# Performance work log

Hardware: AMD Instinct MI355X
Metric: run time of the kernel (lower is better)

Reference implementation:

```python
import jax, jax.numpy as jnp
import numpy as np

B, S, H, MAX_STEP = 128, 1024, 256, 10
NEG_INF = -1e8


def setup_inputs() -> dict:
    key = jax.random.key(0)
    ks = jax.random.split(key, 16)
    sc = 0.05
    return {
        "s0": jax.random.normal(ks[0], (B, H), jnp.float32),
        "h0": jax.random.normal(ks[1], (B, H), jnp.float32),
        "doc_encoding": jax.random.normal(ks[2], (B, S, H), jnp.float32),
        "W_ih": jax.random.normal(ks[3], (3 * H, H), jnp.float32) * sc,
        "W_hh": jax.random.normal(ks[4], (3 * H, H), jnp.float32) * sc,
        "b_ih": jax.random.normal(ks[5], (3 * H,), jnp.float32) * sc,
        "b_hh": jax.random.normal(ks[6], (3 * H,), jnp.float32) * sc,
        "Wq": jax.random.normal(ks[7], (H, H), jnp.float32) * sc,
        "bq": jax.random.normal(ks[8], (H,), jnp.float32) * sc,
        "Wd": jax.random.normal(ks[9], (H, H), jnp.float32) * sc,
        "bd": jax.random.normal(ks[10], (H,), jnp.float32) * sc,
        "Ws": jax.random.normal(ks[11], (1, H), jnp.float32) * sc,
        "bs": jax.random.normal(ks[12], (1,), jnp.float32) * sc,
        "tgt": jax.random.randint(ks[13], (B, MAX_STEP), 0, S, jnp.int64 if jax.config.jax_enable_x64 else jnp.int32),
        "sent_length": jax.random.randint(ks[14], (B,), 1, S + 1, jnp.int64 if jax.config.jax_enable_x64 else jnp.int32),
    }


def reference(s0, h0, doc_encoding, W_ih, W_hh, b_ih, b_hh, Wq, bq, Wd, bd, Ws, bs, tgt, sent_length):
    batch, sent_len, hid = doc_encoding.shape
    # padding mask: 1 where position >= doc length
    mask = (jnp.arange(sent_len)[None, :] >= sent_length[:, None]).astype(doc_encoding.dtype)  # [B,S]
    # precomputed attention keys: linear_d(context)
    precompute = jnp.einsum('bsh,kh->bsk', doc_encoding, Wd) + bd  # [B,S,H]
    # teacher-forced indices (original maps -1 -> 0)
    tgt_idx = jnp.where(tgt == -1, 0, tgt)  # [B,T]
    batch_ar = jnp.arange(batch)

    def gru_cell(x, h):
        gi = x @ W_ih.T + b_ih  # [B,3H]
        gh = h @ W_hh.T + b_hh
        i_r, i_z, i_n = jnp.split(gi, 3, axis=-1)
        h_r, h_z, h_n = jnp.split(gh, 3, axis=-1)
        r = jax.nn.sigmoid(i_r + h_r)
        z = jax.nn.sigmoid(i_z + h_z)
        n = jnp.tanh(i_n + r * h_n)
        return (1.0 - z) * n + z * h

    def step(carry, idx_t):
        cur_input, h = carry
        h = gru_cell(cur_input, h)
        target = h @ Wq.T + bq  # [B,H]
        energy = jnp.squeeze(jnp.tanh(precompute + target[:, None, :]) @ Ws.T, -1) + bs[0]  # [B,S]
        energy = energy * (1.0 - mask) + mask * NEG_INF
        cur_next = doc_encoding[batch_ar, idx_t]  # hard-attention gather [B,H]
        return (cur_next, h), energy

    _, all_score = jax.lax.scan(step, (s0, h0), tgt_idx.T)  # [T,B,S]
    return all_score, mask
```

## Files before the change

kernel.cpp:

```cpp
#include <hip/hip_runtime.h>

typedef unsigned short ushort_t;
typedef unsigned int uint_t;
typedef __attribute__((ext_vector_type(8))) short short8;
typedef __attribute__((ext_vector_type(4))) float f32x4;

#define B_   128
#define S_   1024
#define H_   256
#define T_   10
#define NEG_INF_ -1e8f

static __device__ __forceinline__ ushort_t f2bf(float x) {
    unsigned int u = __float_as_uint(x);
    unsigned int r = u + 0x7FFFu + ((u >> 16) & 1u);
    return (ushort_t)(r >> 16);
}
static __device__ __forceinline__ float bflo(uint_t w) {
    return __uint_as_float(w << 16);
}
static __device__ __forceinline__ float bfhi(uint_t w) {
    return __uint_as_float(w & 0xFFFF0000u);
}
static __device__ __forceinline__ float sigf(float x) {
    return 1.0f / (1.0f + __expf(-x));
}
static __device__ __forceinline__ float tanh_acc(float x) {
    return 2.0f / (1.0f + __expf(-2.0f * x)) - 1.0f;
}
static __device__ __forceinline__ float tanh_fast(float x) {
    float u = x * x;
    float p = fmaf(0.019063f, u, -0.18852f);
    p = fmaf(p, u, 0.93106f);
    float r = x * p;
    return __builtin_amdgcn_fmed3f(r, -1.0f, 1.0f);
}
static __device__ __forceinline__ short8 pack_bf8(float4 a, float4 b) {
    short8 r;
    r[0] = (short)f2bf(a.x); r[1] = (short)f2bf(a.y);
    r[2] = (short)f2bf(a.z); r[3] = (short)f2bf(a.w);
    r[4] = (short)f2bf(b.x); r[5] = (short)f2bf(b.y);
    r[6] = (short)f2bf(b.z); r[7] = (short)f2bf(b.w);
    return r;
}

__global__ void prep_transpose(const float* __restrict__ W_ih,
                               const float* __restrict__ W_hh,
                               const float* __restrict__ Wq,
                               uint_t* __restrict__ planes) {
    __shared__ float lds[64][65];
    const int p = blockIdx.x >> 4, tile = blockIdx.x & 15;
    const int j0 = (tile >> 2) * 64, c0 = (tile & 3) * 64;
    const float* src;
    if (p < 3)      src = W_ih + (size_t)p * 65536;
    else if (p < 6) src = W_hh + (size_t)(p - 3) * 65536;
    else            src = Wq;
    uint_t* dst = planes + (size_t)p * 32768;
    const int tid = threadIdx.x;
#pragma unroll
    for (int p4 = 0; p4 < 4; ++p4) {
        int i = p4 * 256 + tid;
        int jj = i >> 4, cc4 = (i & 15) * 4;
        float4 v = *((const float4*)&src[(size_t)(j0 + jj) * 256 + c0 + cc4]);
        lds[jj][cc4]     = v.x;
        lds[jj][cc4 + 1] = v.y;
        lds[jj][cc4 + 2] = v.z;
        lds[jj][cc4 + 3] = v.w;
    }
    __syncthreads();
#pragma unroll
    for (int p8 = 0; p8 < 8; ++p8) {
        int i = p8 * 256 + tid;
        int c2 = i >> 6, j = i & 63;
        float lo = lds[j][c2 * 2], hi = lds[j][c2 * 2 + 1];
        uint_t val = (uint_t)f2bf(lo) | ((uint_t)f2bf(hi) << 16);
        dst[(size_t)(c0 / 2 + c2) * 256 + j0 + j] = val;
    }
}

__global__ void prep_small(const float* __restrict__ Wd, const int* __restrict__ slen,
                           ushort_t* __restrict__ Wd_bf, float* __restrict__ out_mask,
                           float* __restrict__ out_score) {
    int i = blockIdx.x * 256 + threadIdx.x;
    if (i < 65536) { Wd_bf[i] = f2bf(Wd[i]); return; }
    i -= 65536;
    if (i < B_ * S_) {
        int b = i >> 10, s = i & 1023;
        out_mask[i] = (s >= slen[b]) ? 1.0f : 0.0f;
        return;
    }
    i -= B_ * S_;
    int bs = i & (B_ * S_ - 1);
    int b = bs >> 10, s = bs & 1023;
    if (s >= slen[b]) out_score[i] = NEG_INF_;
}

__global__ __launch_bounds__(1024) void build_tiles(const int* __restrict__ slen,
                                                    int* __restrict__ tlist,
                                                    int* __restrict__ tcount) {
    const int tid = threadIdx.x;
    const int b = tid >> 3, st = tid & 7;
    const bool active = (st * 128) < slen[b];
    unsigned long long m = __ballot(active);
    const int lane = tid & 63, wv = tid >> 6;
    __shared__ int wbase[16];
    if (lane == 0) wbase[wv] = __popcll(m);
    __syncthreads();
    if (tid == 0) {
        int s = 0;
#pragma unroll
        for (int i = 0; i < 16; ++i) { int c = wbase[i]; wbase[i] = s; s += c; }
        *tcount = s;
    }
    __syncthreads();
    if (active) {
        unsigned long long below = (lane == 0) ? 0ull : (m << (64 - lane));
        int pos = wbase[wv] + __popcll(below);
        tlist[pos] = tid;
    }
}

__global__ __launch_bounds__(512) void gru_all(
        const float* __restrict__ s0, const float* __restrict__ h0,
        const float* __restrict__ doc, const int* __restrict__ tgt,
        const uint_t* __restrict__ planes, const float* __restrict__ b_ih,
        const float* __restrict__ b_hh, const float* __restrict__ bq,
        float* __restrict__ targets) {
    __shared__ float xs[T_][256];
    __shared__ float hs[256];
    __shared__ float pr[256], pz[256], pn[256], pq[256];
    const int b = blockIdx.x;
    const int tid = threadIdx.x;
    const int j = tid & 255, half = tid >> 8;

    const uint_t* ihr = planes;
    const uint_t* ihz = planes + 32768;
    const uint_t* ihn = planes + 2 * 32768;
    const uint_t* hhr = planes + 3 * 32768;
    const uint_t* hhz = planes + 4 * 32768;
    const uint_t* hhn = planes + 5 * 32768;
    const uint_t* qT  = planes + 6 * 32768;

    for (int i = tid; i < 640; i += 512) {
        int t = i >> 6, c4 = i & 63;
        const float* src;
        if (t == 0) src = s0 + (size_t)b * H_;
        else {
            int idx = tgt[b * T_ + t - 1];
            if (idx < 0) idx = 0;
            src = doc + ((size_t)b * S_ + idx) * H_;
        }
        ((float4*)&xs[t][0])[c4] = ((const float4*)src)[c4];
    }
    if (half == 0) hs[j] = h0[(size_t)b * H_ + j];
    const float bhr = b_hh[j], bhz = b_hh[j + 256], bhn = b_hh[j + 512];
    const float bqj = bq[j];
    const float bihr = b_ih[j], bihz = b_ih[j + 256], bihn = b_ih[j + 512];
    __syncthreads();

    float g_r[5], g_z[5], g_n[5];
#pragma unroll
    for (int u = 0; u < 5; ++u) { g_r[u] = bihr; g_z[u] = bihz; g_n[u] = bihn; }
    const int tbase = half * 5;
#pragma unroll 1
    for (int bb = 0; bb < 16; ++bb) {
        uint_t wr8[8], wz8[8], wn8[8];
#pragma unroll
        for (int v = 0; v < 8; ++v) {
            int c2 = bb * 8 + v;
            wr8[v] = ihr[c2 * 256 + j];
            wz8[v] = ihz[c2 * 256 + j];
            wn8[v] = ihn[c2 * 256 + j];
        }
#pragma unroll
        for (int v = 0; v < 8; ++v) {
            int c2 = bb * 8 + v;
            float wr0 = bflo(wr8[v]), wr1 = bfhi(wr8[v]);
            float wz0 = bflo(wz8[v]), wz1 = bfhi(wz8[v]);
            float wn0 = bflo(wn8[v]), wn1 = bfhi(wn8[v]);
#pragma unroll
            for (int u = 0; u < 5; ++u) {
                float2 x2 = *((const float2*)&xs[tbase + u][c2 * 2]);
                g_r[u] = fmaf(wr0, x2.x, g_r[u]); g_r[u] = fmaf(wr1, x2.y, g_r[u]);
                g_z[u] = fmaf(wz0, x2.x, g_z[u]); g_z[u] = fmaf(wz1, x2.y, g_z[u]);
                g_n[u] = fmaf(wn0, x2.x, g_n[u]); g_n[u] = fmaf(wn1, x2.y, g_n[u]);
            }
        }
    }

    const int c2base = half * 64;
    const uint_t* hhr_h = hhr + (size_t)c2base * 256 + j;
    const uint_t* hhz_h = hhz + (size_t)c2base * 256 + j;
    const uint_t* hhn_h = hhn + (size_t)c2base * 256 + j;
    const uint_t* qT_h  = qT  + (size_t)c2base * 256 + j;

#pragma unroll
    for (int t = 0; t < T_; ++t) {
        const bool holder = (half == (t >= 5 ? 1 : 0));
        const int u = (t < 5) ? t : t - 5;
        float ar = 0.f, az = 0.f, an = 0.f;
#pragma unroll 1
        for (int bb = 0; bb < 8; ++bb) {
            uint_t wr8[8], wz8[8], wn8[8];
#pragma unroll
            for (int v = 0; v < 8; ++v) {
                int c2i = bb * 8 + v;
                wr8[v] = hhr_h[c2i * 256];
                wz8[v] = hhz_h[c2i * 256];
                wn8[v] = hhn_h[c2i * 256];
            }
#pragma unroll
            for (int v = 0; v < 8; ++v) {
                int c2i = bb * 8 + v;
                float2 h2 = *((const float2*)&hs[(c2base + c2i) * 2]);
                ar = fmaf(bflo(wr8[v]), h2.x, ar); ar = fmaf(bfhi(wr8[v]), h2.y, ar);
                az = fmaf(bflo(wz8[v]), h2.x, az); az = fmaf(bfhi(wz8[v]), h2.y, az);
                an = fmaf(bflo(wn8[v]), h2.x, an); an = fmaf(bfhi(wn8[v]), h2.y, an);
            }
        }
        if (!holder) { pr[j] = ar; pz[j] = az; pn[j] = an; }
        __syncthreads();
        if (holder) {
            float art = ar + pr[j] + bhr;
            float azt = az + pz[j] + bhz;
            float ant = an + pn[j] + bhn;
            float r = sigf(g_r[u] + art);
            float z = sigf(g_z[u] + azt);
            float n = tanh_acc(fmaf(r, ant, g_n[u]));
            float hold = hs[j];
            hs[j] = fmaf(z, hold - n, n);
        }
        __syncthreads();
        float q = 0.f;
#pragma unroll 1
        for (int bb = 0; bb < 4; ++bb) {
            uint_t wq16[16];
#pragma unroll
            for (int v = 0; v < 16; ++v)
                wq16[v] = qT_h[(bb * 16 + v) * 256];
#pragma unroll
            for (int v = 0; v < 16; ++v) {
                int c2i = bb * 16 + v;
                float2 h2 = *((const float2*)&hs[(c2base + c2i) * 2]);
                q = fmaf(bflo(wq16[v]), h2.x, q); q = fmaf(bfhi(wq16[v]), h2.y, q);
            }
        }
        if (!holder) pq[j] = q;
        __syncthreads();
        if (holder) targets[((size_t)t * B_ + b) * H_ + j] = q + pq[j] + bqj;
    }
}

__global__ __launch_bounds__(256, 3) void energy_kernel(
        const float* __restrict__ doc, const ushort_t* __restrict__ Wd_bf,
        const float* __restrict__ targets, const float* __restrict__ bd,
        const float* __restrict__ Ws, const float* __restrict__ bs,
        const int* __restrict__ slenp, const int* __restrict__ tlist,
        const int* __restrict__ tcount, float* __restrict__ out) {
    __shared__ float tg[T_][256];
    __shared__ float ws_l[256], bd_l[256];
    const int bid = blockIdx.x;
    if (bid >= *tcount) return;
    const int tile = tlist[bid];
    const int b = tile >> 3, st = tile & 7;
    const int tid = threadIdx.x;

    const int slen = slenp[b];

    for (int i = tid; i < 640; i += 256) {
        int t = i >> 6, k4 = i & 63;
        ((float4*)&tg[t][0])[k4] = *((const float4*)&targets[((size_t)t * B_ + b) * H_ + k4 * 4]);
    }
    if (tid < 64) ((float4*)ws_l)[tid] = ((const float4*)Ws)[tid];
    else if (tid < 128) ((float4*)bd_l)[tid - 64] = ((const float4*)bd)[tid - 64];

    const int lane = tid & 63, w = tid >> 6;
    const int r16 = lane & 15, g = lane >> 4;

    const int s0_loc = st * 128 + w * 16 + r16;
    const float* drow0 = doc + ((size_t)b * S_ + s0_loc) * H_ + g * 8;
    const float* drow1 = drow0 + (size_t)64 * H_;
    short8 bdoc0[8], bdoc1[8];
#pragma unroll
    for (int ks = 0; ks < 8; ++ks) {
        float4 v0 = *((const float4*)(drow0 + ks * 32));
        float4 v1 = *((const float4*)(drow0 + ks * 32 + 4));
        bdoc0[ks] = pack_bf8(v0, v1);
        float4 u0 = *((const float4*)(drow1 + ks * 32));
        float4 u1 = *((const float4*)(drow1 + ks * 32 + 4));
        bdoc1[ks] = pack_bf8(u0, u1);
    }
    __syncthreads();

    float e0[T_], e1[T_];
#pragma unroll
    for (int t = 0; t < T_; ++t) { e0[t] = 0.f; e1[t] = 0.f; }

    const ushort_t* wbase = Wd_bf + (size_t)r16 * H_ + g * 8;
    const int kq = g * 4;

    short8 awd[8];
#pragma unroll
    for (int ks = 0; ks < 8; ++ks) awd[ks] = *((const short8*)(wbase + ks * 32));

#pragma unroll 1
    for (int nt = 0; nt < 16; ++nt) {
        const int k0 = nt * 16 + kq;

        short8 awn[8];
        if (nt < 15) {
            const ushort_t* wnext = wbase + (size_t)((nt + 1) * 16) * H_;
#pragma unroll
            for (int ks = 0; ks < 8; ++ks) awn[ks] = *((const short8*)(wnext + ks * 32));
        }

        f32x4 bd4 = *((const f32x4*)&bd_l[k0]);
        f32x4 a00 = bd4;
        f32x4 a01 = {0.f, 0.f, 0.f, 0.f};
        f32x4 a10 = bd4;
        f32x4 a11 = {0.f, 0.f, 0.f, 0.f};
#pragma unroll
        for (int ks = 0; ks < 4; ++ks) {
            a00 = __builtin_amdgcn_mfma_f32_16x16x32_bf16(awd[ks],     bdoc0[ks],     a00, 0, 0, 0);
            a01 = __builtin_amdgcn_mfma_f32_16x16x32_bf16(awd[ks + 4], bdoc0[ks + 4], a01, 0, 0, 0);
            a10 = __builtin_amdgcn_mfma_f32_16x16x32_bf16(awd[ks],     bdoc1[ks],     a10, 0, 0, 0);
            a11 = __builtin_amdgcn_mfma_f32_16x16x32_bf16(awd[ks + 4], bdoc1[ks + 4], a11, 0, 0, 0);
        }
        f32x4 pA = a00 + a01;
        f32x4 pB = a10 + a11;
        f32x4 ws4 = *((const f32x4*)&ws_l[k0]);
#pragma unroll
        for (int t = 0; t < T_; ++t) {
            f32x4 tg4 = *((const f32x4*)&tg[t][k0]);
#pragma unroll
            for (int rr = 0; rr < 4; ++rr) {
                e0[t] = fmaf(tanh_fast(pA[rr] + tg4[rr]), ws4[rr], e0[t]);
                e1[t] = fmaf(tanh_fast(pB[rr] + tg4[rr]), ws4[rr], e1[t]);
            }
        }

#pragma unroll
        for (int ks = 0; ks < 8; ++ks) awd[ks] = awn[ks];
    }

#pragma unroll
    for (int t = 0; t < T_; ++t) {
        e0[t] += __shfl_xor(e0[t], 16);
        e0[t] += __shfl_xor(e0[t], 32);
        e1[t] += __shfl_xor(e1[t], 16);
        e1[t] += __shfl_xor(e1[t], 32);
    }

    const float bs0 = bs[0];
    const bool pad0 = (s0_loc >= slen);
    const bool pad1 = (s0_loc + 64 >= slen);
    float* obase = out + (size_t)b * S_ + s0_loc;
#pragma unroll
    for (int tt = g; tt < T_; tt += 4) {
        if (!pad0) obase[(size_t)tt * B_ * S_]      = e0[tt] + bs0;
        if (!pad1) obase[(size_t)tt * B_ * S_ + 64] = e1[tt] + bs0;
    }
}

extern "C" void kernel_launch(void* const* d_in, const int* in_sizes, int n_in,
                              void* d_out, int out_size, void* d_ws, size_t ws_size,
                              hipStream_t stream) {
    (void)in_sizes; (void)n_in; (void)out_size; (void)ws_size;
    const float* s0   = (const float*)d_in[0];
    const float* h0   = (const float*)d_in[1];
    const float* doc  = (const float*)d_in[2];
    const float* W_ih = (const float*)d_in[3];
    const float* W_hh = (const float*)d_in[4];
    const float* b_ih = (const float*)d_in[5];
    const float* b_hh = (const float*)d_in[6];
    const float* Wq   = (const float*)d_in[7];
    const float* bq   = (const float*)d_in[8];
    const float* Wd   = (const float*)d_in[9];
    const float* bd   = (const float*)d_in[10];
    const float* Ws   = (const float*)d_in[11];
    const float* bs   = (const float*)d_in[12];
    const int*   tgt  = (const int*)d_in[13];
    const int*   slen = (const int*)d_in[14];

    float* out_score = (float*)d_out;
    float* out_mask  = out_score + T_ * B_ * S_;

    char* ws = (char*)d_ws;
    uint_t*   planes  = (uint_t*)(ws + 0);
    ushort_t* Wd_bf   = (ushort_t*)(ws + 917504);
    float*    targets = (float*)(ws + 1048576);
    int*      tlist   = (int*)(ws + 2359296);
    int*      tcount  = (int*)(ws + 2363392);

    prep_transpose<<<112, 256, 0, stream>>>(W_ih, W_hh, Wq, planes);
    prep_small<<<5888, 256, 0, stream>>>(Wd, slen, Wd_bf, out_mask, out_score);
    build_tiles<<<1, 1024, 0, stream>>>(slen, tlist, tcount);
    gru_all<<<128, 512, 0, stream>>>(s0, h0, doc, tgt, planes, b_ih, b_hh, bq, targets);
    energy_kernel<<<1024, 256, 0, stream>>>(doc, Wd_bf, targets, bd, Ws, bs, slen,
                                            tlist, tcount, out_score);
}
```

Measured before the change: 161.6 us.

## Split GRU into batched input-projection, recurrent-only kernel, and batched query projection

Moves the non-recurrent input-gate GEMM (x·W_ih) and the per-step query projection (h·Wq) out of the sequential per-batch GRU kernel into separate batched kernels over all T*B rows, using fp32 W_ih directly. The recurrent kernel now runs 1024 threads per batch, splitting the hidden-to-hidden reduction four ways, and only writes h per step. This shortens the serial critical path and spreads the independent matmuls over more blocks. The cost is two extra kernel launches and round trips of gi_all and h_all through global memory.

```diff
diff --git a/kernel.cpp b/kernel.cpp
--- a/kernel.cpp
+++ b/kernel.cpp
@@ -44,17 +44,13 @@
     return r;
 }
 
-__global__ void prep_transpose(const float* __restrict__ W_ih,
-                               const float* __restrict__ W_hh,
+__global__ void prep_transpose(const float* __restrict__ W_hh,
                                const float* __restrict__ Wq,
                                uint_t* __restrict__ planes) {
     __shared__ float lds[64][65];
     const int p = blockIdx.x >> 4, tile = blockIdx.x & 15;
     const int j0 = (tile >> 2) * 64, c0 = (tile & 3) * 64;
-    const float* src;
-    if (p < 3)      src = W_ih + (size_t)p * 65536;
-    else if (p < 6) src = W_hh + (size_t)(p - 3) * 65536;
-    else            src = Wq;
+    const float* src = (p < 3) ? (W_hh + (size_t)p * 65536) : Wq;
     uint_t* dst = planes + (size_t)p * 32768;
     const int tid = threadIdx.x;
 #pragma unroll
@@ -120,29 +116,16 @@
     }
 }
 
-__global__ __launch_bounds__(512) void gru_all(
-        const float* __restrict__ s0, const float* __restrict__ h0,
-        const float* __restrict__ doc, const int* __restrict__ tgt,
-        const uint_t* __restrict__ planes, const float* __restrict__ b_ih,
-        const float* __restrict__ b_hh, const float* __restrict__ bq,
-        float* __restrict__ targets) {
-    __shared__ float xs[T_][256];
-    __shared__ float hs[256];
-    __shared__ float pr[256], pz[256], pn[256], pq[256];
-    const int b = blockIdx.x;
+__global__ void prep_gi(const float* __restrict__ s0, const float* __restrict__ doc,
+                        const int* __restrict__ tgt, const float* __restrict__ W_ih,
+                        const float* __restrict__ b_ih, float* __restrict__ gi_all) {
+    __shared__ float xs[8][256];
+    const int r0 = blockIdx.x * 8;
     const int tid = threadIdx.x;
-    const int j = tid & 255, half = tid >> 8;
-
-    const uint_t* ihr = planes;
-    const uint_t* ihz = planes + 32768;
-    const uint_t* ihn = planes + 2 * 32768;
-    const uint_t* hhr = planes + 3 * 32768;
-    const uint_t* hhz = planes + 4 * 32768;
-    const uint_t* hhn = planes + 5 * 32768;
-    const uint_t* qT  = planes + 6 * 32768;
-
-    for (int i = tid; i < 640; i += 512) {
-        int t = i >> 6, c4 = i & 63;
+    for (int i = tid; i < 512; i += 256) {
+        int row = i >> 6, c4 = i & 63;
+        int r = r0 + row;
+        int t = r >> 7, b = r & 127;
         const float* src;
         if (t == 0) src = s0 + (size_t)b * H_;
         else {
@@ -150,57 +133,63 @@
             if (idx < 0) idx = 0;
             src = doc + ((size_t)b * S_ + idx) * H_;
         }
-        ((float4*)&xs[t][0])[c4] = ((const float4*)src)[c4];
-    }
-    if (half == 0) hs[j] = h0[(size_t)b * H_ + j];
+        *((float4*)&xs[row][c4 * 4]) = ((const float4*)src)[c4];
+    }
+    __syncthreads();
+    const int j = tid;
+    float acc[8][3];
+#pragma unroll
+    for (int r = 0; r < 8; ++r) { acc[r][0] = 0.f; acc[r][1] = 0.f; acc[r][2] = 0.f; }
+    const float4* w0p = (const float4*)(W_ih + (size_t)j * H_);
+    const float4* w1p = (const float4*)(W_ih + (size_t)(j + 256) * H_);
+    const float4* w2p = (const float4*)(W_ih + (size_t)(j + 512) * H_);
+    for (int c4 = 0; c4 < 64; ++c4) {
+        float4 w0 = w0p[c4], w1 = w1p[c4], w2 = w2p[c4];
+#pragma unroll
+        for (int r = 0; r < 8; ++r) {
+            float4 x4 = *((const float4*)&xs[r][c4 * 4]);
+            acc[r][0] = fmaf(w0.x, x4.x, acc[r][0]); acc[r][0] = fmaf(w0.y, x4.y, acc[r][0]);
+            acc[r][0] = fmaf(w0.z, x4.z, acc[r][0]); acc[r][0] = fmaf(w0.w, x4.w, acc[r][0]);
+            acc[r][1] = fmaf(w1.x, x4.x, acc[r][1]); acc[r][1] = fmaf(w1.y, x4.y, acc[r][1]);
+            acc[r][1] = fmaf(w1.z, x4.z, acc[r][1]); acc[r][1] = fmaf(w1.w, x4.w, acc[r][1]);
+            acc[r][2] = fmaf(w2.x, x4.x, acc[r][2]); acc[r][2] = fmaf(w2.y, x4.y, acc[r][2]);
+            acc[r][2] = fmaf(w2.z, x4.z, acc[r][2]); acc[r][2] = fmaf(w2.w, x4.w, acc[r][2]);
+        }
+    }
+#pragma unroll
+    for (int r = 0; r < 8; ++r)
+#pragma unroll
+        for (int g = 0; g < 3; ++g)
+            gi_all[(size_t)(r0 + r) * 768 + g * 256 + j] = acc[r][g] + b_ih[g * 256 + j];
+}
+
+__global__ __launch_bounds__(1024) void gru_h(
+        const float* __restrict__ h0, const uint_t* __restrict__ planes,
+        const float* __restrict__ b_hh, const float* __restrict__ gi_all,
+        float* __restrict__ h_all) {
+    __shared__ float hs[256];
+    __shared__ float pp[3][3][256];
+    const int b = blockIdx.x;
+    const int tid = threadIdx.x;
+    const int j = tid & 255, qt = tid >> 8;
+
+    const uint_t* hhr = planes;
+    const uint_t* hhz = planes + 32768;
+    const uint_t* hhn = planes + 2 * 32768;
+
+    if (qt == 0) hs[j] = h0[(size_t)b * H_ + j];
     const float bhr = b_hh[j], bhz = b_hh[j + 256], bhn = b_hh[j + 512];
-    const float bqj = bq[j];
-    const float bihr = b_ih[j], bihz = b_ih[j + 256], bihn = b_ih[j + 512];
-    __syncthreads();
-
-    float g_r[5], g_z[5], g_n[5];
-#pragma unroll
-    for (int u = 0; u < 5; ++u) { g_r[u] = bihr; g_z[u] = bihz; g_n[u] = bihn; }
-    const int tbase = half * 5;
-#pragma unroll 1
-    for (int bb = 0; bb < 16; ++bb) {
-        uint_t wr8[8], wz8[8], wn8[8];
-#pragma unroll
-        for (int v = 0; v < 8; ++v) {
-            int c2 = bb * 8 + v;
-            wr8[v] = ihr[c2 * 256 + j];
-            wz8[v] = ihz[c2 * 256 + j];
-            wn8[v] = ihn[c2 * 256 + j];
-        }
-#pragma unroll
-        for (int v = 0; v < 8; ++v) {
-            int c2 = bb * 8 + v;
-            float wr0 = bflo(wr8[v]), wr1 = bfhi(wr8[v]);
-            float wz0 = bflo(wz8[v]), wz1 = bfhi(wz8[v]);
-            float wn0 = bflo(wn8[v]), wn1 = bfhi(wn8[v]);
-#pragma unroll
-            for (int u = 0; u < 5; ++u) {
-                float2 x2 = *((const float2*)&xs[tbase + u][c2 * 2]);
-                g_r[u] = fmaf(wr0, x2.x, g_r[u]); g_r[u] = fmaf(wr1, x2.y, g_r[u]);
-                g_z[u] = fmaf(wz0, x2.x, g_z[u]); g_z[u] = fmaf(wz1, x2.y, g_z[u]);
-                g_n[u] = fmaf(wn0, x2.x, g_n[u]); g_n[u] = fmaf(wn1, x2.y, g_n[u]);
-            }
-        }
-    }
-
-    const int c2base = half * 64;
+
+    const int c2base = qt * 32;
     const uint_t* hhr_h = hhr + (size_t)c2base * 256 + j;
     const uint_t* hhz_h = hhz + (size_t)c2base * 256 + j;
     const uint_t* hhn_h = hhn + (size_t)c2base * 256 + j;
-    const uint_t* qT_h  = qT  + (size_t)c2base * 256 + j;
-
-#pragma unroll
+    __syncthreads();
+
     for (int t = 0; t < T_; ++t) {
-        const bool holder = (half == (t >= 5 ? 1 : 0));
-        const int u = (t < 5) ? t : t - 5;
         float ar = 0.f, az = 0.f, an = 0.f;
 #pragma unroll 1
-        for (int bb = 0; bb < 8; ++bb) {
+        for (int bb = 0; bb < 4; ++bb) {
             uint_t wr8[8], wz8[8], wn8[8];
 #pragma unroll
             for (int v = 0; v < 8; ++v) {
@@ -218,37 +207,58 @@
                 an = fmaf(bflo(wn8[v]), h2.x, an); an = fmaf(bfhi(wn8[v]), h2.y, an);
             }
         }
-        if (!holder) { pr[j] = ar; pz[j] = az; pn[j] = an; }
+        if (qt) { pp[qt - 1][0][j] = ar; pp[qt - 1][1][j] = az; pp[qt - 1][2][j] = an; }
         __syncthreads();
-        if (holder) {
-            float art = ar + pr[j] + bhr;
-            float azt = az + pz[j] + bhz;
-            float ant = an + pn[j] + bhn;
-            float r = sigf(g_r[u] + art);
-            float z = sigf(g_z[u] + azt);
-            float n = tanh_acc(fmaf(r, ant, g_n[u]));
-            float hold = hs[j];
-            hs[j] = fmaf(z, hold - n, n);
+        if (qt == 0) {
+            ar += pp[0][0][j] + pp[1][0][j] + pp[2][0][j] + bhr;
+            az += pp[0][1][j] + pp[1][1][j] + pp[2][1][j] + bhz;
+            an += pp[0][2][j] + pp[1][2][j] + pp[2][2][j] + bhn;
+            const float* gi = gi_all + ((size_t)t * B_ + b) * 768;
+            float r = sigf(gi[j] + ar);
+            float z = sigf(gi[j + 256] + az);
+            float n = tanh_acc(fmaf(r, an, gi[j + 512]));
+            float hnew = fmaf(z, hs[j] - n, n);
+            hs[j] = hnew;
+            h_all[((size_t)t * B_ + b) * H_ + j] = hnew;
         }
         __syncthreads();
-        float q = 0.f;
+    }
+}
+
+__global__ void q_proj(const float* __restrict__ h_all, const uint_t* __restrict__ planes,
+                       const float* __restrict__ bq, float* __restrict__ targets) {
+    __shared__ float hsh[8][256];
+    const int r0 = blockIdx.x * 8;
+    const int tid = threadIdx.x, j = tid;
+    const uint_t* qT = planes + 3 * 32768;
+    for (int i = tid; i < 512; i += 256) {
+        int row = i >> 6, c4 = i & 63;
+        *((float4*)&hsh[row][c4 * 4]) = ((const float4*)(h_all + (size_t)(r0 + row) * H_))[c4];
+    }
+    __syncthreads();
+    const float bqj = bq[j];
+    float acc[8];
+#pragma unroll
+    for (int r = 0; r < 8; ++r) acc[r] = bqj;
 #pragma unroll 1
-        for (int bb = 0; bb < 4; ++bb) {
-            uint_t wq16[16];
-#pragma unroll
-            for (int v = 0; v < 16; ++v)
-                wq16[v] = qT_h[(bb * 16 + v) * 256];
-#pragma unroll
-            for (int v = 0; v < 16; ++v) {
-                int c2i = bb * 16 + v;
-                float2 h2 = *((const float2*)&hs[(c2base + c2i) * 2]);
-                q = fmaf(bflo(wq16[v]), h2.x, q); q = fmaf(bfhi(wq16[v]), h2.y, q);
+    for (int bb = 0; bb < 16; ++bb) {
+        uint_t w8[8];
+#pragma unroll
+        for (int v = 0; v < 8; ++v) w8[v] = qT[(size_t)(bb * 8 + v) * 256 + j];
+#pragma unroll
+        for (int v = 0; v < 8; ++v) {
+            int c2 = bb * 8 + v;
+            float lo = bflo(w8[v]), hi = bfhi(w8[v]);
+#pragma unroll
+            for (int r = 0; r < 8; ++r) {
+                acc[r] = fmaf(lo, hsh[r][c2 * 2],     acc[r]);
+                acc[r] = fmaf(hi, hsh[r][c2 * 2 + 1], acc[r]);
             }
         }
-        if (!holder) pq[j] = q;
-        __syncthreads();
-        if (holder) targets[((size_t)t * B_ + b) * H_ + j] = q + pq[j] + bqj;
-    }
+    }
+#pragma unroll
+    for (int r = 0; r < 8; ++r)
+        targets[(size_t)(r0 + r) * H_ + j] = acc[r];
 }
 
 __global__ __launch_bounds__(256, 3) void energy_kernel(
@@ -387,15 +397,19 @@
 
     char* ws = (char*)d_ws;
     uint_t*   planes  = (uint_t*)(ws + 0);
-    ushort_t* Wd_bf   = (ushort_t*)(ws + 917504);
-    float*    targets = (float*)(ws + 1048576);
-    int*      tlist   = (int*)(ws + 2359296);
-    int*      tcount  = (int*)(ws + 2363392);
-
-    prep_transpose<<<112, 256, 0, stream>>>(W_ih, W_hh, Wq, planes);
+    ushort_t* Wd_bf   = (ushort_t*)(ws + 524288);
+    float*    targets = (float*)(ws + 655360);
+    float*    gi_all  = (float*)(ws + 1966080);
+    float*    h_all   = (float*)(ws + 5898240);
+    int*      tlist   = (int*)(ws + 7208960);
+    int*      tcount  = (int*)(ws + 7213056);
+
+    prep_transpose<<<64, 256, 0, stream>>>(W_hh, Wq, planes);
     prep_small<<<5888, 256, 0, stream>>>(Wd, slen, Wd_bf, out_mask, out_score);
     build_tiles<<<1, 1024, 0, stream>>>(slen, tlist, tcount);
-    gru_all<<<128, 512, 0, stream>>>(s0, h0, doc, tgt, planes, b_ih, b_hh, bq, targets);
+    prep_gi<<<160, 256, 0, stream>>>(s0, doc, tgt, W_ih, b_ih, gi_all);
+    gru_h<<<128, 1024, 0, stream>>>(h0, planes, b_hh, gi_all, h_all);
+    q_proj<<<160, 256, 0, stream>>>(h_all, planes, bq, targets);
     energy_kernel<<<1024, 256, 0, stream>>>(doc, Wd_bf, targets, bd, Ws, bs, slen,
                                             tlist, tcount, out_score);
 }
```

Result: slower. 179.8 us (+11.3%).

## Stage precompute tile in LDS and split energy epilogue across threads with smaller tiles

Applied to the files above, without the earlier changes.

The energy kernel now uses 64-row sequence tiles instead of 128, doubling the grid and making the tile list finer. Each block first computes the full Wd·doc precompute tile with MFMA into padded LDS (about 77 KB of dynamic shared memory). A second phase then spreads the tanh/Ws reduction over threads, with four threads per row each handling a quarter of the hidden dimension, so the MFMA layout no longer serialises the epilogue. The large LDS footprint limits occupancy to about one or two blocks per CU, and the change adds a barrier and an LDS round-trip in exchange for less skipped padding and better balance of the tanh work.

```diff
diff --git a/kernel.cpp b/kernel.cpp
--- a/kernel.cpp
+++ b/kernel.cpp
@@ -10,6 +10,7 @@
 #define H_   256
 #define T_   10
 #define NEG_INF_ -1e8f
+#define PRE_STRIDE 260
 
 static __device__ __forceinline__ ushort_t f2bf(float x) {
     unsigned int u = __float_as_uint(x);
@@ -99,24 +100,29 @@
                                                     int* __restrict__ tlist,
                                                     int* __restrict__ tcount) {
     const int tid = threadIdx.x;
-    const int b = tid >> 3, st = tid & 7;
-    const bool active = (st * 128) < slen[b];
-    unsigned long long m = __ballot(active);
     const int lane = tid & 63, wv = tid >> 6;
-    __shared__ int wbase[16];
-    if (lane == 0) wbase[wv] = __popcll(m);
+    __shared__ int wcnt[32], woff[32];
+    const bool a0 = ((tid & 15) * 64) < slen[tid >> 4];
+    unsigned long long m0 = __ballot(a0);
+    const int t2 = 1024 + tid;
+    const bool a1 = ((t2 & 15) * 64) < slen[t2 >> 4];
+    unsigned long long m1 = __ballot(a1);
+    if (lane == 0) { wcnt[wv] = __popcll(m0); wcnt[16 + wv] = __popcll(m1); }
     __syncthreads();
     if (tid == 0) {
         int s = 0;
 #pragma unroll
-        for (int i = 0; i < 16; ++i) { int c = wbase[i]; wbase[i] = s; s += c; }
+        for (int i = 0; i < 32; ++i) { woff[i] = s; s += wcnt[i]; }
         *tcount = s;
     }
     __syncthreads();
-    if (active) {
-        unsigned long long below = (lane == 0) ? 0ull : (m << (64 - lane));
-        int pos = wbase[wv] + __popcll(below);
-        tlist[pos] = tid;
+    if (a0) {
+        unsigned long long below = (lane == 0) ? 0ull : (m0 << (64 - lane));
+        tlist[woff[wv] + __popcll(below)] = tid;
+    }
+    if (a1) {
+        unsigned long long below = (lane == 0) ? 0ull : (m1 << (64 - lane));
+        tlist[woff[16 + wv] + __popcll(below)] = t2;
     }
 }
 
@@ -251,25 +257,29 @@
     }
 }
 
-__global__ __launch_bounds__(256, 3) void energy_kernel(
+__global__ __launch_bounds__(256) void energy_kernel(
         const float* __restrict__ doc, const ushort_t* __restrict__ Wd_bf,
         const float* __restrict__ targets, const float* __restrict__ bd,
         const float* __restrict__ Ws, const float* __restrict__ bs,
         const int* __restrict__ slenp, const int* __restrict__ tlist,
         const int* __restrict__ tcount, float* __restrict__ out) {
-    __shared__ float tg[T_][256];
-    __shared__ float ws_l[256], bd_l[256];
+    extern __shared__ char smem[];
+    float* pre_l = (float*)smem;
+    float* tg_l  = (float*)(smem + 66560);
+    float* ws_l  = (float*)(smem + 76800);
+    float* bd_l  = (float*)(smem + 77824);
+
     const int bid = blockIdx.x;
     if (bid >= *tcount) return;
     const int tile = tlist[bid];
-    const int b = tile >> 3, st = tile & 7;
+    const int b = tile >> 4, st = tile & 15;
     const int tid = threadIdx.x;
-
     const int slen = slenp[b];
 
     for (int i = tid; i < 640; i += 256) {
         int t = i >> 6, k4 = i & 63;
-        ((float4*)&tg[t][0])[k4] = *((const float4*)&targets[((size_t)t * B_ + b) * H_ + k4 * 4]);
+        ((float4*)&tg_l[t * 256])[k4] =
+            *((const float4*)&targets[((size_t)t * B_ + b) * H_ + k4 * 4]);
     }
     if (tid < 64) ((float4*)ws_l)[tid] = ((const float4*)Ws)[tid];
     else if (tid < 128) ((float4*)bd_l)[tid - 64] = ((const float4*)bd)[tid - 64];
@@ -277,27 +287,19 @@
     const int lane = tid & 63, w = tid >> 6;
     const int r16 = lane & 15, g = lane >> 4;
 
-    const int s0_loc = st * 128 + w * 16 + r16;
-    const float* drow0 = doc + ((size_t)b * S_ + s0_loc) * H_ + g * 8;
-    const float* drow1 = drow0 + (size_t)64 * H_;
-    short8 bdoc0[8], bdoc1[8];
+    const int srow = w * 16 + r16;
+    const float* drow = doc + ((size_t)b * S_ + st * 64 + srow) * H_ + g * 8;
+    short8 bdoc[8];
 #pragma unroll
     for (int ks = 0; ks < 8; ++ks) {
-        float4 v0 = *((const float4*)(drow0 + ks * 32));
-        float4 v1 = *((const float4*)(drow0 + ks * 32 + 4));
-        bdoc0[ks] = pack_bf8(v0, v1);
-        float4 u0 = *((const float4*)(drow1 + ks * 32));
-        float4 u1 = *((const float4*)(drow1 + ks * 32 + 4));
-        bdoc1[ks] = pack_bf8(u0, u1);
-    }
-    __syncthreads();
-
-    float e0[T_], e1[T_];
-#pragma unroll
-    for (int t = 0; t < T_; ++t) { e0[t] = 0.f; e1[t] = 0.f; }
+        float4 v0 = *((const float4*)(drow + ks * 32));
+        float4 v1 = *((const float4*)(drow + ks * 32 + 4));
+        bdoc[ks] = pack_bf8(v0, v1);
+    }
+    __syncthreads();
 
     const ushort_t* wbase = Wd_bf + (size_t)r16 * H_ + g * 8;
-    const int kq = g * 4;
+    const int kq4 = g * 4;
 
     short8 awd[8];
 #pragma unroll
@@ -305,60 +307,59 @@
 
 #pragma unroll 1
     for (int nt = 0; nt < 16; ++nt) {
-        const int k0 = nt * 16 + kq;
-
         short8 awn[8];
         if (nt < 15) {
             const ushort_t* wnext = wbase + (size_t)((nt + 1) * 16) * H_;
 #pragma unroll
             for (int ks = 0; ks < 8; ++ks) awn[ks] = *((const short8*)(wnext + ks * 32));
         }
-
-        f32x4 bd4 = *((const f32x4*)&bd_l[k0]);
-        f32x4 a00 = bd4;
-        f32x4 a01 = {0.f, 0.f, 0.f, 0.f};
-        f32x4 a10 = bd4;
-        f32x4 a11 = {0.f, 0.f, 0.f, 0.f};
+        f32x4 a0 = *((const f32x4*)&bd_l[nt * 16 + kq4]);
+        f32x4 a1 = {0.f, 0.f, 0.f, 0.f};
 #pragma unroll
         for (int ks = 0; ks < 4; ++ks) {
-            a00 = __builtin_amdgcn_mfma_f32_16x16x32_bf16(awd[ks],     bdoc0[ks],     a00, 0, 0, 0);
-            a01 = __builtin_amdgcn_mfma_f32_16x16x32_bf16(awd[ks + 4], bdoc0[ks + 4], a01, 0, 0, 0);
-            a10 = __builtin_amdgcn_mfma_f32_16x16x32_bf16(awd[ks],     bdoc1[ks],     a10, 0, 0, 0);
-            a11 = __builtin_amdgcn_mfma_f32_16x16x32_bf16(awd[ks + 4], bdoc1[ks + 4], a11, 0, 0, 0);
-        }
-        f32x4 pA = a00 + a01;
-        f32x4 pB = a10 + a11;
-        f32x4 ws4 = *((const f32x4*)&ws_l[k0]);
+            a0 = __builtin_amdgcn_mfma_f32_16x16x32_bf16(awd[ks],     bdoc[ks],     a0, 0, 0, 0);
+            a1 = __builtin_amdgcn_mfma_f32_16x16x32_bf16(awd[ks + 4], bdoc[ks + 4], a1, 0, 0, 0);
+        }
+        f32x4 pre4 = a0 + a1;
+        *((f32x4*)&pre_l[srow * PRE_STRIDE + nt * 16 + kq4]) = pre4;
+#pragma unroll
+        for (int ks = 0; ks < 8; ++ks) awd[ks] = awn[ks];
+    }
+    __syncthreads();
+
+    const int s = tid >> 2, kq = tid & 3;
+    float e[T_];
+#pragma unroll
+    for (int t = 0; t < T_; ++t) e[t] = 0.f;
+
+    const float* prow = &pre_l[s * PRE_STRIDE + kq * 64];
+#pragma unroll 1
+    for (int kk = 0; kk < 16; ++kk) {
+        const int K = kq * 64 + kk * 4;
+        f32x4 x4  = *((const f32x4*)(prow + kk * 4));
+        f32x4 ws4 = *((const f32x4*)&ws_l[K]);
 #pragma unroll
         for (int t = 0; t < T_; ++t) {
-            f32x4 tg4 = *((const f32x4*)&tg[t][k0]);
-#pragma unroll
-            for (int rr = 0; rr < 4; ++rr) {
-                e0[t] = fmaf(tanh_fast(pA[rr] + tg4[rr]), ws4[rr], e0[t]);
-                e1[t] = fmaf(tanh_fast(pB[rr] + tg4[rr]), ws4[rr], e1[t]);
-            }
-        }
-
-#pragma unroll
-        for (int ks = 0; ks < 8; ++ks) awd[ks] = awn[ks];
+            f32x4 tg4 = *((const f32x4*)&tg_l[t * 256 + K]);
+#pragma unroll
+            for (int rr = 0; rr < 4; ++rr)
+                e[t] = fmaf(tanh_fast(x4[rr] + tg4[rr]), ws4[rr], e[t]);
+        }
     }
 
 #pragma unroll
     for (int t = 0; t < T_; ++t) {
-        e0[t] += __shfl_xor(e0[t], 16);
-        e0[t] += __shfl_xor(e0[t], 32);
-        e1[t] += __shfl_xor(e1[t], 16);
-        e1[t] += __shfl_xor(e1[t], 32);
-    }
-
-    const float bs0 = bs[0];
-    const bool pad0 = (s0_loc >= slen);
-    const bool pad1 = (s0_loc + 64 >= slen);
-    float* obase = out + (size_t)b * S_ + s0_loc;
-#pragma unroll
-    for (int tt = g; tt < T_; tt += 4) {
-        if (!pad0) obase[(size_t)tt * B_ * S_]      = e0[tt] + bs0;
-        if (!pad1) obase[(size_t)tt * B_ * S_ + 64] = e1[tt] + bs0;
+        e[t] += __shfl_xor(e[t], 1);
+        e[t] += __shfl_xor(e[t], 2);
+    }
+
+    const int s_glob = st * 64 + s;
+    if (kq == 0 && s_glob < slen) {
+        const float bs0 = bs[0];
+        float* obase = out + (size_t)b * S_ + s_glob;
+#pragma unroll
+        for (int t = 0; t < T_; ++t)
+            obase[(size_t)t * B_ * S_] = e[t] + bs0;
     }
 }
 
@@ -390,12 +391,12 @@
     ushort_t* Wd_bf   = (ushort_t*)(ws + 917504);
     float*    targets = (float*)(ws + 1048576);
     int*      tlist   = (int*)(ws + 2359296);
-    int*      tcount  = (int*)(ws + 2363392);
+    int*      tcount  = (int*)(ws + 2367488);
 
     prep_transpose<<<112, 256, 0, stream>>>(W_ih, W_hh, Wq, planes);
     prep_small<<<5888, 256, 0, stream>>>(Wd, slen, Wd_bf, out_mask, out_score);
     build_tiles<<<1, 1024, 0, stream>>>(slen, tlist, tcount);
     gru_all<<<128, 512, 0, stream>>>(s0, h0, doc, tgt, planes, b_ih, b_hh, bq, targets);
-    energy_kernel<<<1024, 256, 0, stream>>>(doc, Wd_bf, targets, bd, Ws, bs, slen,
-                                            tlist, tcount, out_score);
-}
+    energy_kernel<<<2048, 256, 78848, stream>>>(doc, Wd_bf, targets, bd, Ws, bs, slen,
+                                                tlist, tcount, out_score);
+}
```

Measured after the change: 204.2 us. 1.26x slower.
